# Kernel optimization log

Hardware: AMD Instinct MI355X
Metric: run time of the kernel (lower is better)

The kernel has to match this reference:

```python
import jax, jax.numpy as jnp
import numpy as np
import math

B, M, C, H = 4, 2048, 512, 8
DQK = C // 4 // H  # 16 per-head query/key dim


def setup_inputs() -> dict:
    key = jax.random.key(0)
    ks = jax.random.split(key, 8)
    s = 0.02
    return {
        "x": jax.random.normal(ks[0], (B, M, C), dtype=jnp.float32),
        "mask": jax.random.randint(ks[1], (B, M), 0, 2, dtype=jnp.int32),
        "Wq": jax.random.normal(ks[2], (C, C // 4), dtype=jnp.float32) * s,
        "bq": jnp.zeros((C // 4,), dtype=jnp.float32),
        "Wk": jax.random.normal(ks[3], (C, C // 4), dtype=jnp.float32) * s,
        "bk": jnp.zeros((C // 4,), dtype=jnp.float32),
        "Wv": jax.random.normal(ks[4], (C, C), dtype=jnp.float32) * s,
        "bv": jnp.zeros((C,), dtype=jnp.float32),
        "gamma": jnp.ones((1,), dtype=jnp.float32),
    }


def reference(x, mask, Wq, bq, Wk, bk, Wv, bv, gamma):
    b, m, c = x.shape
    # projections, split heads: q/k -> (B, H, M, DQK), v -> (B, H, M, C//H)
    q = (x @ Wq + bq).reshape(b, m, H, -1).transpose(0, 2, 1, 3)
    k = (x @ Wk + bk).reshape(b, m, H, -1).transpose(0, 2, 1, 3)
    v = (x @ Wv + bv).reshape(b, m, H, -1).transpose(0, 2, 1, 3)
    scale = 1.0 / math.sqrt(q.shape[-1])
    scores = jnp.einsum('bhmd,bhnd->bhmn', q, k) * scale
    beta = jax.nn.softmax(jax.nn.relu(scores), axis=-1)  # act='relu' pre-softmax
    # att_drop = 0.0 -> identity
    mf = mask.astype(x.dtype)[:, None, None, :]  # (B,1,1,M)
    beta = beta * mf
    beta = beta / (beta.sum(-1, keepdims=True) + 1e-12)
    o = gamma * jnp.einsum('bhmn,bhnd->bhmd', beta, v)  # (B,H,M,C//H)
    return o.transpose(0, 2, 1, 3).reshape(b, m, c)
```

## Files before the change

kernel.cpp:

```cpp
#include <hip/hip_runtime.h>
#include <hip/hip_bf16.h>

#define MSEQ 2048

typedef __attribute__((ext_vector_type(8))) short short8;
typedef __attribute__((ext_vector_type(4))) short short4v;
typedef __attribute__((ext_vector_type(4))) float f32x4;

static __device__ __forceinline__ short bf16b(float f) {
    __hip_bfloat16 h = __float2bfloat16(f);
    return *reinterpret_cast<short*>(&h);
}

static __device__ __forceinline__ float fast_exp2(float x) {
    float r;
    asm("v_exp_f32 %0, %1" : "=v"(r) : "v"(x));
    return r;
}

static __device__ __forceinline__ f32x4 mfma16(short4v a, short4v b, f32x4 c) {
    return __builtin_amdgcn_mfma_f32_16x16x16bf16_1k(a, b, c, 0, 0, 0);
}

static __device__ __forceinline__ void gl_lds16(const void* g, void* l) {
    __builtin_amdgcn_global_load_lds(
        (const __attribute__((address_space(1))) unsigned int*)g,
        (__attribute__((address_space(3))) unsigned int*)l, 16, 0, 0);
}

__global__ __launch_bounds__(256) void prep_kernel(
    const float* __restrict__ x, unsigned short* __restrict__ xb,
    const float* __restrict__ Wq, const float* __restrict__ Wk,
    const float* __restrict__ Wv, unsigned short* __restrict__ WT,
    const int* __restrict__ mask, unsigned short* __restrict__ maskbf)
{
    __shared__ unsigned short Ts[64*72];
    const int bid = blockIdx.x;
    const int t = threadIdx.x;

    if (bid < 2048) {
        const size_t i = ((size_t)bid * 256 + t) * 8;
        const float4 a = *(const float4*)(x + i);
        const float4 b = *(const float4*)(x + i + 4);
        short8 o;
        o[0]=bf16b(a.x); o[1]=bf16b(a.y); o[2]=bf16b(a.z); o[3]=bf16b(a.w);
        o[4]=bf16b(b.x); o[5]=bf16b(b.y); o[6]=bf16b(b.z); o[7]=bf16b(b.w);
        *(short8*)(xb + i) = o;
        return;
    }
    if (bid == 2144) {
        #pragma unroll
        for (int j = 0; j < 8; ++j) {
            const int4 m4 = *(const int4*)(mask + (t*8 + j)*4);
            short4v o;
            o[0]=bf16b((float)m4.x); o[1]=bf16b((float)m4.y);
            o[2]=bf16b((float)m4.z); o[3]=bf16b((float)m4.w);
            *(short4v*)(maskbf + (t*8 + j)*4) = o;
        }
        return;
    }
    const int idx = bid - 2048;
    const int nt = idx >> 3;
    const int kt = idx & 7;
    const int k0 = kt*64;

    const float* W; int ld, n0;
    if (nt < 2)      { W = Wq; ld = 128; n0 = nt*64; }
    else if (nt < 4) { W = Wk; ld = 128; n0 = (nt-2)*64; }
    else             { W = Wv; ld = 512; n0 = (nt-4)*64; }

    #pragma unroll
    for (int s = 0; s < 4; ++s) {
        const int lin = s*256 + t;
        const int krow = lin >> 4, ng = lin & 15;
        const float4 v = *(const float4*)(W + (size_t)(k0+krow)*ld + n0 + ng*4);
        Ts[(ng*4+0)*72 + krow] = (unsigned short)bf16b(v.x);
        Ts[(ng*4+1)*72 + krow] = (unsigned short)bf16b(v.y);
        Ts[(ng*4+2)*72 + krow] = (unsigned short)bf16b(v.z);
        Ts[(ng*4+3)*72 + krow] = (unsigned short)bf16b(v.w);
    }
    __syncthreads();
    #pragma unroll
    for (int s = 0; s < 2; ++s) {
        const int lin = s*256 + t;
        const int nrow = lin >> 3, kg = lin & 7;
        *(short8*)(WT + (size_t)(nt*64 + nrow)*512 + k0 + kg*8) = *(const short8*)&Ts[nrow*72 + kg*8];
    }
}

__global__ __launch_bounds__(256, 3) void proj_mfma(
    const unsigned short* __restrict__ xb, const unsigned short* __restrict__ WT,
    const float* __restrict__ bq, const float* __restrict__ bk, const float* __restrict__ bv,
    const int* __restrict__ mask,
    unsigned short* __restrict__ Qb, unsigned short* __restrict__ Kb, unsigned short* __restrict__ Vt)
{
    const int nt = blockIdx.x;
    const int r0 = blockIdx.y * 64;
    const int n0 = nt * 128;
    const int t = threadIdx.x, w = t >> 6, lane = t & 63, l15 = lane & 15, quad = lane >> 4;
    const int qh = w >> 1, chh = w & 1;

    __shared__ short smem[12288];
    short* As = smem;
    short* Bs = smem + 4096;

    f32x4 acc[2][4];
    #pragma unroll
    for (int i = 0; i < 2; ++i)
        #pragma unroll
        for (int j = 0; j < 4; ++j) acc[i][j] = {0.f,0.f,0.f,0.f};

    const int arow = lane >> 2, akg = lane & 3;

#define PROJ_STAGE(BUFI, KK) {                                                          \
    gl_lds16(xb + (size_t)(r0 + w*16 + arow)*512 + (KK) + akg*8,                        \
             (char*)As + (BUFI)*4096 + w*1024);                                         \
    gl_lds16(WT + (size_t)(n0 + w*16 + arow)*512 + (KK) + akg*8,                        \
             (char*)Bs + (BUFI)*8192 + w*1024);                                         \
    gl_lds16(WT + (size_t)(n0 + 64 + w*16 + arow)*512 + (KK) + akg*8,                   \
             (char*)Bs + (BUFI)*8192 + 4096 + w*1024);                                  \
}

    PROJ_STAGE(0, 0)
    __syncthreads();

    #pragma unroll 1
    for (int kp = 0; kp < 16; ++kp) {
        const int cur = kp & 1;
        if (kp < 15) PROJ_STAGE(cur ^ 1, (kp+1)*32)
        short8 Af[2], Bf[4];
        #pragma unroll
        for (int i = 0; i < 2; ++i)
            Af[i] = *(const short8*)&As[cur*2048 + (qh*32 + i*16 + l15)*32 + quad*8];
        #pragma unroll
        for (int j = 0; j < 4; ++j)
            Bf[j] = *(const short8*)&Bs[cur*4096 + (chh*64 + j*16 + l15)*32 + quad*8];
        #pragma unroll
        for (int i = 0; i < 2; ++i)
            #pragma unroll
            for (int j = 0; j < 4; ++j)
                acc[i][j] = __builtin_amdgcn_mfma_f32_16x16x32_bf16(Af[i], Bf[j], acc[i][j], 0, 0, 0);
        __syncthreads();
    }

    const float* bias = (nt == 0) ? bq : (nt == 1) ? bk : (bv + (nt-2)*128);
    const float kscale = (nt == 1) ? 0.36067376022224085f : 1.0f;
    float bj[4];
    #pragma unroll
    for (int j = 0; j < 4; ++j) bj[j] = bias[chh*64 + j*16 + l15];

    const int bb = r0 >> 11, key0 = r0 & 2047;
    short* Ts = smem;
    if (nt < 2) {
        #pragma unroll
        for (int i = 0; i < 2; ++i)
            #pragma unroll
            for (int j = 0; j < 4; ++j)
                #pragma unroll
                for (int r = 0; r < 4; ++r)
                    Ts[(qh*32 + i*16 + quad*4 + r)*136 + chh*64 + j*16 + l15] =
                        bf16b((acc[i][j][r] + bj[j]) * kscale);
    } else {
        float mv[2][4];
        #pragma unroll
        for (int i = 0; i < 2; ++i)
            #pragma unroll
            for (int r = 0; r < 4; ++r)
                mv[i][r] = (float)mask[bb*MSEQ + key0 + qh*32 + i*16 + quad*4 + r];
        #pragma unroll
        for (int i = 0; i < 2; ++i)
            #pragma unroll
            for (int j = 0; j < 4; ++j)
                #pragma unroll
                for (int r = 0; r < 4; ++r)
                    Ts[(chh*64 + j*16 + l15)*72 + qh*32 + i*16 + quad*4 + r] =
                        bf16b((acc[i][j][r] + bj[j]) * mv[i][r]);
    }
    __syncthreads();

    if (nt < 2) {
        unsigned short* Out = (nt == 0) ? Qb : Kb;
        #pragma unroll
        for (int s = 0; s < 4; ++s) {
            const int lin = s*256 + t, row = lin >> 4, seg = lin & 15;
            *(short8*)(Out + (size_t)(r0+row)*128 + seg*8) = *(const short8*)&Ts[row*136 + seg*8];
        }
    } else {
        const int chBase = (nt-2)*128;
        #pragma unroll
        for (int s = 0; s < 4; ++s) {
            const int lin = s*256 + t, row = lin >> 3, seg = lin & 7;
            *(short8*)(Vt + ((size_t)(bb*512 + chBase + row))*MSEQ + key0 + seg*8) =
                *(const short8*)&Ts[row*72 + seg*8];
        }
    }
#undef PROJ_STAGE
}

__global__ __launch_bounds__(256, 4) void attn_mfma(
    const unsigned short* __restrict__ Qb, const unsigned short* __restrict__ Kb,
    const unsigned short* __restrict__ Vt, const unsigned short* __restrict__ maskbf,
    const float* __restrict__ gamma, float* __restrict__ out)
{
    const int bid = blockIdx.y * 32 + blockIdx.x;
    const int lin = (bid & 7) * 128 + (bid >> 3);
    const int mt = lin & 31, bh = lin >> 5;
    const int b  = bh >> 3, h = bh & 7;
    const int m0 = mt * 64;
    const int t  = threadIdx.x;
    const int w = t >> 6, lane = t & 63, l15 = lane & 15, quad = lane >> 4;
    const int mq = m0 + w*16;

    __shared__ __align__(16) short Ks[2][64*16];
    __shared__ __align__(16) short Vs[2][64*64];
    __shared__ __align__(16) short Msb[2][64];

    const short4v qf = *(const short4v*)(Qb + (size_t)(b*MSEQ + mq + l15)*128 + h*16 + quad*4);

    const unsigned short* Kg = Kb + (size_t)(b*MSEQ + (lane>>1))*128 + h*16
                              + (((lane&1) ^ ((lane>>3)&1))*8);
    const int vj0 = 2*w;
    const unsigned short* Vg0 = Vt + (size_t)(b*512 + h*64 + vj0*8 + (lane>>3))*MSEQ
                               + (((lane&7) ^ ((lane>>3)&7)) * 8);
    const unsigned short* Vg1 = Vg0 + (size_t)8*MSEQ;
    const unsigned short* Mgb = maskbf + b*MSEQ + lane*8;

#define ATT_STAGE(BUFI, KN) {                                                       \
    gl_lds16(Vg0 + (KN), &Vs[BUFI][vj0*512]);                                       \
    gl_lds16(Vg1 + (KN), &Vs[BUFI][(vj0+1)*512]);                                   \
    if (w < 2)          gl_lds16(Kg + (size_t)((KN) + w*32)*128, &Ks[BUFI][w*32*16]);\
    else if (lane < 8)  gl_lds16(Mgb + (KN), &Msb[BUFI][0]);                        \
}

    const char* KsB = (const char*)&Ks[0][0];
    const char* VsB = (const char*)&Vs[0][0];
    const char* MsB = (const char*)&Msb[0][0];
    const int kofs = l15*32 + (((quad>>1) ^ ((l15>>2)&1))*16) + (quad&1)*8;
    const int mofs = quad*8;
    int vb[4];
    #pragma unroll
    for (int v = 0; v < 4; ++v) {
        const int ch = v*16 + l15;
        vb[v] = ch*128 + (((quad>>1) ^ (ch&7))*16) + (quad&1)*8;
    }

    f32x4 O[4];
    #pragma unroll
    for (int v = 0; v < 4; ++v) O[v] = {0.f,0.f,0.f,0.f};
    f32x4 WS = {0.f,0.f,0.f,0.f};

    ATT_STAGE(0, 0)
    __syncthreads();

    #pragma unroll 1
    for (int kt = 0; kt < 32; ++kt) {
        const int cur = kt & 1;
        if (kt < 31) ATT_STAGE(cur ^ 1, (kt+1)*64)

        const char* Kc = KsB + cur*2048;
        const char* Vc = VsB + cur*8192;
        const char* Mc = MsB + cur*128;

        #pragma unroll
        for (int s = 0; s < 4; ++s) {
            const short4v kf  = *(const short4v*)(Kc + kofs + s*512);
            const short4v mkf = *(const short4v*)(Mc + mofs + s*32);
            f32x4 sc = {0.f,0.f,0.f,0.f};
            sc = mfma16(kf, qf, sc);
            const float w0 = fast_exp2(fmaxf(sc[0], 0.f));
            const float w1 = fast_exp2(fmaxf(sc[1], 0.f));
            const float w2 = fast_exp2(fmaxf(sc[2], 0.f));
            const float w3 = fast_exp2(fmaxf(sc[3], 0.f));
            short4v pf;
            pf[0]=bf16b(w0); pf[1]=bf16b(w1); pf[2]=bf16b(w2); pf[3]=bf16b(w3);
            WS = mfma16(pf, mkf, WS);
            #pragma unroll
            for (int v = 0; v < 4; ++v) {
                const short4v vf = *(const short4v*)(Vc + (vb[v] ^ (s*32)));
                O[v] = mfma16(pf, vf, O[v]);
            }
        }
        __syncthreads();
    }

    const float g = gamma[0];
    float inv[4];
    #pragma unroll
    for (int r = 0; r < 4; ++r) inv[r] = g / fmaxf(WS[r], 1e-20f);

    float* op = out + (size_t)(b*MSEQ + mq + quad*4)*512 + h*64 + l15;
    #pragma unroll
    for (int r = 0; r < 4; ++r) {
        op[(size_t)r*512 +  0] = O[0][r] * inv[r];
        op[(size_t)r*512 + 16] = O[1][r] * inv[r];
        op[(size_t)r*512 + 32] = O[2][r] * inv[r];
        op[(size_t)r*512 + 48] = O[3][r] * inv[r];
    }
#undef ATT_STAGE
}

extern "C" void kernel_launch(void* const* d_in, const int* in_sizes, int n_in,
                              void* d_out, int out_size, void* d_ws, size_t ws_size,
                              hipStream_t stream) {
    const float* x     = (const float*)d_in[0];
    const int*   mask  = (const int*)  d_in[1];
    const float* Wq    = (const float*)d_in[2];
    const float* bq    = (const float*)d_in[3];
    const float* Wk    = (const float*)d_in[4];
    const float* bk    = (const float*)d_in[5];
    const float* Wv    = (const float*)d_in[6];
    const float* bv    = (const float*)d_in[7];
    const float* gamma = (const float*)d_in[8];
    float* outp = (float*)d_out;

    unsigned short* xb = (unsigned short*)d_ws;
    unsigned short* WT = xb + (size_t)8192*512;
    unsigned short* Qb = WT + (size_t)768*512;
    unsigned short* Kb = Qb + (size_t)8192*128;
    unsigned short* Vt = Kb + (size_t)8192*128;
    unsigned short* maskbf = Vt + (size_t)2048*MSEQ;

    prep_kernel<<<2145, 256, 0, stream>>>(x, xb, Wq, Wk, Wv, WT, mask, maskbf);
    proj_mfma<<<dim3(6, 128), 256, 0, stream>>>(xb, WT, bq, bk, bv, mask, Qb, Kb, Vt);
    attn_mfma<<<dim3(32, 32), 256, 0, stream>>>(Qb, Kb, Vt, maskbf, gamma, outp);
}
```

Baseline: 152.8 us.

## Use 128-query attention tiles with 512 threads, splitting V channels across wave pairs

The attention kernel now processes 128 queries per block with 8 waves instead of 64 queries with 4 waves. Each wave pair covers 32 queries and splits the 64 V channels in half. Each K/V tile loaded into LDS is therefore reused across twice as many queries, halving global K/V traffic per query. K and mask fragments are also hoisted out of the inner loop. The cost is that each wave recomputes the score MFMA and exp for its queries, duplicating that work across channel halves, and there are fewer, larger blocks.

```diff
diff --git a/kernel.cpp b/kernel.cpp
--- a/kernel.cpp
+++ b/kernel.cpp
@@ -197,39 +197,40 @@
 #undef PROJ_STAGE
 }
 
-__global__ __launch_bounds__(256, 4) void attn_mfma(
+__global__ __launch_bounds__(512, 4) void attn_mfma(
     const unsigned short* __restrict__ Qb, const unsigned short* __restrict__ Kb,
     const unsigned short* __restrict__ Vt, const unsigned short* __restrict__ maskbf,
     const float* __restrict__ gamma, float* __restrict__ out)
 {
-    const int bid = blockIdx.y * 32 + blockIdx.x;
-    const int lin = (bid & 7) * 128 + (bid >> 3);
-    const int mt = lin & 31, bh = lin >> 5;
+    const int bid = blockIdx.y * 16 + blockIdx.x;
+    const int lin = (bid & 7) * 64 + (bid >> 3);
+    const int mt = lin & 15, bh = lin >> 4;
     const int b  = bh >> 3, h = bh & 7;
-    const int m0 = mt * 64;
+    const int m0 = mt * 128;
     const int t  = threadIdx.x;
     const int w = t >> 6, lane = t & 63, l15 = lane & 15, quad = lane >> 4;
-    const int mq = m0 + w*16;
+    const int qg2 = w >> 1, chh = w & 1;
+    const int mq = m0 + qg2*32;
 
     __shared__ __align__(16) short Ks[2][64*16];
     __shared__ __align__(16) short Vs[2][64*64];
     __shared__ __align__(16) short Msb[2][64];
 
-    const short4v qf = *(const short4v*)(Qb + (size_t)(b*MSEQ + mq + l15)*128 + h*16 + quad*4);
+    short4v qf[2];
+    #pragma unroll
+    for (int g = 0; g < 2; ++g)
+        qf[g] = *(const short4v*)(Qb + (size_t)(b*MSEQ + mq + g*16 + l15)*128 + h*16 + quad*4);
 
     const unsigned short* Kg = Kb + (size_t)(b*MSEQ + (lane>>1))*128 + h*16
                               + (((lane&1) ^ ((lane>>3)&1))*8);
-    const int vj0 = 2*w;
-    const unsigned short* Vg0 = Vt + (size_t)(b*512 + h*64 + vj0*8 + (lane>>3))*MSEQ
-                               + (((lane&7) ^ ((lane>>3)&7)) * 8);
-    const unsigned short* Vg1 = Vg0 + (size_t)8*MSEQ;
+    const unsigned short* Vg = Vt + (size_t)(b*512 + h*64 + w*8 + (lane>>3))*MSEQ
+                              + (((lane&7) ^ ((lane>>3)&7)) * 8);
     const unsigned short* Mgb = maskbf + b*MSEQ + lane*8;
 
-#define ATT_STAGE(BUFI, KN) {                                                       \
-    gl_lds16(Vg0 + (KN), &Vs[BUFI][vj0*512]);                                       \
-    gl_lds16(Vg1 + (KN), &Vs[BUFI][(vj0+1)*512]);                                   \
-    if (w < 2)          gl_lds16(Kg + (size_t)((KN) + w*32)*128, &Ks[BUFI][w*32*16]);\
-    else if (lane < 8)  gl_lds16(Mgb + (KN), &Msb[BUFI][0]);                        \
+#define ATT_STAGE(BUFI, KN) {                                                        \
+    gl_lds16(Vg + (KN), &Vs[BUFI][w*512]);                                           \
+    if (w < 2)                   gl_lds16(Kg + (size_t)((KN) + w*32)*128, &Ks[BUFI][w*32*16]); \
+    else if (w == 2 && lane < 8) gl_lds16(Mgb + (KN), &Msb[BUFI][0]);                \
 }
 
     const char* KsB = (const char*)&Ks[0][0];
@@ -237,17 +238,19 @@
     const char* MsB = (const char*)&Msb[0][0];
     const int kofs = l15*32 + (((quad>>1) ^ ((l15>>2)&1))*16) + (quad&1)*8;
     const int mofs = quad*8;
-    int vb[4];
-    #pragma unroll
-    for (int v = 0; v < 4; ++v) {
-        const int ch = v*16 + l15;
+    int vb[2];
+    #pragma unroll
+    for (int v = 0; v < 2; ++v) {
+        const int ch = chh*32 + v*16 + l15;
         vb[v] = ch*128 + (((quad>>1) ^ (ch&7))*16) + (quad&1)*8;
     }
 
-    f32x4 O[4];
-    #pragma unroll
-    for (int v = 0; v < 4; ++v) O[v] = {0.f,0.f,0.f,0.f};
-    f32x4 WS = {0.f,0.f,0.f,0.f};
+    f32x4 O[2][2];
+    #pragma unroll
+    for (int g = 0; g < 2; ++g)
+        #pragma unroll
+        for (int v = 0; v < 2; ++v) O[g][v] = {0.f,0.f,0.f,0.f};
+    f32x4 WS[2] = {{0.f,0.f,0.f,0.f},{0.f,0.f,0.f,0.f}};
 
     ATT_STAGE(0, 0)
     __syncthreads();
@@ -261,40 +264,47 @@
         const char* Vc = VsB + cur*8192;
         const char* Mc = MsB + cur*128;
 
+        short4v kfs[4], mkfs[4];
         #pragma unroll
         for (int s = 0; s < 4; ++s) {
-            const short4v kf  = *(const short4v*)(Kc + kofs + s*512);
-            const short4v mkf = *(const short4v*)(Mc + mofs + s*32);
-            f32x4 sc = {0.f,0.f,0.f,0.f};
-            sc = mfma16(kf, qf, sc);
-            const float w0 = fast_exp2(fmaxf(sc[0], 0.f));
-            const float w1 = fast_exp2(fmaxf(sc[1], 0.f));
-            const float w2 = fast_exp2(fmaxf(sc[2], 0.f));
-            const float w3 = fast_exp2(fmaxf(sc[3], 0.f));
-            short4v pf;
-            pf[0]=bf16b(w0); pf[1]=bf16b(w1); pf[2]=bf16b(w2); pf[3]=bf16b(w3);
-            WS = mfma16(pf, mkf, WS);
-            #pragma unroll
-            for (int v = 0; v < 4; ++v) {
-                const short4v vf = *(const short4v*)(Vc + (vb[v] ^ (s*32)));
-                O[v] = mfma16(pf, vf, O[v]);
+            kfs[s]  = *(const short4v*)(Kc + kofs + s*512);
+            mkfs[s] = *(const short4v*)(Mc + mofs + s*32);
+        }
+
+        #pragma unroll
+        for (int s = 0; s < 4; ++s) {
+            short4v vf[2];
+            #pragma unroll
+            for (int v = 0; v < 2; ++v)
+                vf[v] = *(const short4v*)(Vc + (vb[v] ^ (s*32)));
+            #pragma unroll
+            for (int g = 0; g < 2; ++g) {
+                f32x4 sc = {0.f,0.f,0.f,0.f};
+                sc = mfma16(kfs[s], qf[g], sc);
+                const float w0 = fast_exp2(fmaxf(sc[0], 0.f));
+                const float w1 = fast_exp2(fmaxf(sc[1], 0.f));
+                const float w2 = fast_exp2(fmaxf(sc[2], 0.f));
+                const float w3 = fast_exp2(fmaxf(sc[3], 0.f));
+                short4v pf;
+                pf[0]=bf16b(w0); pf[1]=bf16b(w1); pf[2]=bf16b(w2); pf[3]=bf16b(w3);
+                WS[g] = mfma16(pf, mkfs[s], WS[g]);
+                O[g][0] = mfma16(pf, vf[0], O[g][0]);
+                O[g][1] = mfma16(pf, vf[1], O[g][1]);
             }
         }
         __syncthreads();
     }
 
-    const float g = gamma[0];
-    float inv[4];
-    #pragma unroll
-    for (int r = 0; r < 4; ++r) inv[r] = g / fmaxf(WS[r], 1e-20f);
-
-    float* op = out + (size_t)(b*MSEQ + mq + quad*4)*512 + h*64 + l15;
-    #pragma unroll
-    for (int r = 0; r < 4; ++r) {
-        op[(size_t)r*512 +  0] = O[0][r] * inv[r];
-        op[(size_t)r*512 + 16] = O[1][r] * inv[r];
-        op[(size_t)r*512 + 32] = O[2][r] * inv[r];
-        op[(size_t)r*512 + 48] = O[3][r] * inv[r];
+    const float gm = gamma[0];
+    #pragma unroll
+    for (int g = 0; g < 2; ++g) {
+        #pragma unroll
+        for (int r = 0; r < 4; ++r) {
+            const float inv = gm / fmaxf(WS[g][r], 1e-20f);
+            float* op = out + (size_t)(b*MSEQ + mq + g*16 + quad*4 + r)*512 + h*64 + chh*32 + l15;
+            op[0]  = O[g][0][r] * inv;
+            op[16] = O[g][1][r] * inv;
+        }
     }
 #undef ATT_STAGE
 }
@@ -322,5 +332,5 @@
 
     prep_kernel<<<2145, 256, 0, stream>>>(x, xb, Wq, Wk, Wv, WT, mask, maskbf);
     proj_mfma<<<dim3(6, 128), 256, 0, stream>>>(xb, WT, bq, bk, bv, mask, Qb, Kb, Vt);
-    attn_mfma<<<dim3(32, 32), 256, 0, stream>>>(Qb, Kb, Vt, maskbf, gamma, outp);
-}
+    attn_mfma<<<dim3(16, 32), 512, 0, stream>>>(Qb, Kb, Vt, maskbf, gamma, outp);
+}
```

After: 172.2 us. 1.13x slower.

## Double attention block to 512 threads and remap proj blocks per XCD

Applied to the files above, without the earlier changes.

The attention kernel now runs 8 waves per block covering 128 query rows, so each staged K/V tile is shared by twice as many queries and each wave loads one V row-group instead of two. The K and mask fragments are loaded up front, and the compute section is wrapped in s_setprio to favour MFMA issue. The projection kernel remaps its block index so row tiles are grouped by XCD for better L2 locality. The cost is fewer blocks (512 instead of 1024) and heavier barriers with 8 waves per block.

```diff
diff --git a/kernel.cpp b/kernel.cpp
--- a/kernel.cpp
+++ b/kernel.cpp
@@ -94,8 +94,10 @@
     const int* __restrict__ mask,
     unsigned short* __restrict__ Qb, unsigned short* __restrict__ Kb, unsigned short* __restrict__ Vt)
 {
-    const int nt = blockIdx.x;
-    const int r0 = blockIdx.y * 64;
+    const int g0 = blockIdx.y * 6 + blockIdx.x;
+    const int xcd = g0 & 7, idx = g0 >> 3;
+    const int nt = idx / 16;
+    const int r0 = (xcd * 16 + (idx & 15)) * 64;
     const int n0 = nt * 128;
     const int t = threadIdx.x, w = t >> 6, lane = t & 63, l15 = lane & 15, quad = lane >> 4;
     const int qh = w >> 1, chh = w & 1;
@@ -197,16 +199,16 @@
 #undef PROJ_STAGE
 }
 
-__global__ __launch_bounds__(256, 4) void attn_mfma(
+__global__ __launch_bounds__(512, 4) void attn_mfma(
     const unsigned short* __restrict__ Qb, const unsigned short* __restrict__ Kb,
     const unsigned short* __restrict__ Vt, const unsigned short* __restrict__ maskbf,
     const float* __restrict__ gamma, float* __restrict__ out)
 {
-    const int bid = blockIdx.y * 32 + blockIdx.x;
-    const int lin = (bid & 7) * 128 + (bid >> 3);
-    const int mt = lin & 31, bh = lin >> 5;
+    const int bid = blockIdx.y * 16 + blockIdx.x;
+    const int lin = (bid & 7) * 64 + (bid >> 3);
+    const int mt = lin & 15, bh = lin >> 4;
     const int b  = bh >> 3, h = bh & 7;
-    const int m0 = mt * 64;
+    const int m0 = mt * 128;
     const int t  = threadIdx.x;
     const int w = t >> 6, lane = t & 63, l15 = lane & 15, quad = lane >> 4;
     const int mq = m0 + w*16;
@@ -219,17 +221,14 @@
 
     const unsigned short* Kg = Kb + (size_t)(b*MSEQ + (lane>>1))*128 + h*16
                               + (((lane&1) ^ ((lane>>3)&1))*8);
-    const int vj0 = 2*w;
-    const unsigned short* Vg0 = Vt + (size_t)(b*512 + h*64 + vj0*8 + (lane>>3))*MSEQ
-                               + (((lane&7) ^ ((lane>>3)&7)) * 8);
-    const unsigned short* Vg1 = Vg0 + (size_t)8*MSEQ;
+    const unsigned short* Vg = Vt + (size_t)(b*512 + h*64 + w*8 + (lane>>3))*MSEQ
+                              + (((lane&7) ^ ((lane>>3)&7)) * 8);
     const unsigned short* Mgb = maskbf + b*MSEQ + lane*8;
 
-#define ATT_STAGE(BUFI, KN) {                                                       \
-    gl_lds16(Vg0 + (KN), &Vs[BUFI][vj0*512]);                                       \
-    gl_lds16(Vg1 + (KN), &Vs[BUFI][(vj0+1)*512]);                                   \
-    if (w < 2)          gl_lds16(Kg + (size_t)((KN) + w*32)*128, &Ks[BUFI][w*32*16]);\
-    else if (lane < 8)  gl_lds16(Mgb + (KN), &Msb[BUFI][0]);                        \
+#define ATT_STAGE(BUFI, KN) {                                                        \
+    gl_lds16(Vg + (KN), &Vs[BUFI][w*512]);                                           \
+    if (w < 2)                   gl_lds16(Kg + (size_t)((KN) + w*32)*128, &Ks[BUFI][w*32*16]); \
+    else if (w == 2 && lane < 8) gl_lds16(Mgb + (KN), &Msb[BUFI][0]);                \
 }
 
     const char* KsB = (const char*)&Ks[0][0];
@@ -261,25 +260,32 @@
         const char* Vc = VsB + cur*8192;
         const char* Mc = MsB + cur*128;
 
+        __builtin_amdgcn_s_setprio(1);
+        short4v kfs[4], mkfs[4];
         #pragma unroll
         for (int s = 0; s < 4; ++s) {
-            const short4v kf  = *(const short4v*)(Kc + kofs + s*512);
-            const short4v mkf = *(const short4v*)(Mc + mofs + s*32);
+            kfs[s]  = *(const short4v*)(Kc + kofs + s*512);
+            mkfs[s] = *(const short4v*)(Mc + mofs + s*32);
+        }
+
+        #pragma unroll
+        for (int s = 0; s < 4; ++s) {
             f32x4 sc = {0.f,0.f,0.f,0.f};
-            sc = mfma16(kf, qf, sc);
+            sc = mfma16(kfs[s], qf, sc);
             const float w0 = fast_exp2(fmaxf(sc[0], 0.f));
             const float w1 = fast_exp2(fmaxf(sc[1], 0.f));
             const float w2 = fast_exp2(fmaxf(sc[2], 0.f));
             const float w3 = fast_exp2(fmaxf(sc[3], 0.f));
             short4v pf;
             pf[0]=bf16b(w0); pf[1]=bf16b(w1); pf[2]=bf16b(w2); pf[3]=bf16b(w3);
-            WS = mfma16(pf, mkf, WS);
+            WS = mfma16(pf, mkfs[s], WS);
             #pragma unroll
             for (int v = 0; v < 4; ++v) {
                 const short4v vf = *(const short4v*)(Vc + (vb[v] ^ (s*32)));
                 O[v] = mfma16(pf, vf, O[v]);
             }
         }
+        __builtin_amdgcn_s_setprio(0);
         __syncthreads();
     }
 
@@ -322,5 +328,5 @@
 
     prep_kernel<<<2145, 256, 0, stream>>>(x, xb, Wq, Wk, Wv, WT, mask, maskbf);
     proj_mfma<<<dim3(6, 128), 256, 0, stream>>>(xb, WT, bq, bk, bv, mask, Qb, Kb, Vt);
-    attn_mfma<<<dim3(32, 32), 256, 0, stream>>>(Qb, Kb, Vt, maskbf, gamma, outp);
-}
+    attn_mfma<<<dim3(16, 32), 512, 0, stream>>>(Qb, Kb, Vt, maskbf, gamma, outp);
+}
```

Result: faster. 149.1 us (-2.5%).
